# Performance work log

Measured on AMD Instinct MI355X. Metric: run time of the kernel, lower is better.

## Reference

```python
import jax, jax.numpy as jnp
import numpy as np

N = 50000      # total nodes (25 graphs x 2000 proteins)
E = 1200000    # total edges
G = 25         # graphs
F_IN = 128     # protein_features
H = 64         # hidden_dim
L = 2          # num_layers


def setup_inputs() -> dict:
    key = jax.random.key(0)
    ks = jax.random.split(key, 24)
    inp = {
        "x": jax.random.normal(ks[0], (N, F_IN), dtype=jnp.float32),
        "edge_attr": jax.random.uniform(ks[1], (E,), dtype=jnp.float32),
        "global_features": jax.random.normal(ks[2], (G, 6), dtype=jnp.float32),
        "edge_index": jax.random.randint(ks[3], (2, E), 0, N, dtype=jnp.int64),
        "batch": (jnp.arange(N, dtype=jnp.int64) // (N // G)),
    }
    s = 0.05
    inp["W_embed"] = jax.random.normal(ks[4], (F_IN, H), dtype=jnp.float32) * s
    inp["b_embed"] = jnp.zeros((H,), dtype=jnp.float32)
    inp["W_glob"] = jax.random.normal(ks[5], (6, H), dtype=jnp.float32) * s
    inp["b_glob"] = jnp.zeros((H,), dtype=jnp.float32)
    # stacked per-layer GATConv params (heads=1)
    inp["lin_W"] = jax.random.normal(ks[6], (L, H, H), dtype=jnp.float32) * s
    inp["att_src"] = jax.random.normal(ks[7], (L, H), dtype=jnp.float32) * s
    inp["att_dst"] = jax.random.normal(ks[8], (L, H), dtype=jnp.float32) * s
    inp["lin_edge_W"] = jax.random.normal(ks[9], (L, 1, H), dtype=jnp.float32) * s
    inp["att_edge"] = jax.random.normal(ks[10], (L, H), dtype=jnp.float32) * s
    inp["gat_bias"] = jnp.zeros((L, H), dtype=jnp.float32)
    inp["W_comb"] = jax.random.normal(ks[11], (2 * H, H), dtype=jnp.float32) * s
    inp["b_comb"] = jnp.zeros((H,), dtype=jnp.float32)
    inp["W_out"] = jax.random.normal(ks[12], (H, 1), dtype=jnp.float32) * s
    inp["b_out"] = jnp.zeros((1,), dtype=jnp.float32)
    return inp


def _forward(x, edge_attr, global_features, W_embed, b_embed, W_glob, b_glob,
             lin_W, att_src, att_dst, lin_edge_W, att_edge, gat_bias,
             W_comb, b_comb, W_out, b_out, edge_index, batch):
    src, dst = edge_index[0], edge_index[1]
    h = x @ W_embed + b_embed                       # [N,H]
    g = global_features @ W_glob + b_glob           # [G,H]
    ea = edge_attr[:, None]                         # [E,1] (edge_attr.unsqueeze(1))
    for l in range(L):
        hs = h @ lin_W[l]                           # [N,H] shared lin_src/lin_dst
        a_src = hs @ att_src[l]                     # [N]
        a_dst = hs @ att_dst[l]                     # [N]
        ef = ea @ lin_edge_W[l]                     # [E,H]
        a_edge = ef @ att_edge[l]                   # [E]
        alpha = jax.nn.leaky_relu(a_src[src] + a_dst[dst] + a_edge, 0.2)
        # segment softmax over incoming edges of each dst node
        m = jax.ops.segment_max(alpha, dst, num_segments=N)
        ex = jnp.exp(alpha - m[dst])
        denom = jax.ops.segment_sum(ex, dst, num_segments=N)
        alpha = ex / (denom[dst] + 1e-16)
        msg = alpha[:, None] * hs[src]              # [E,H]
        h = jax.ops.segment_sum(msg, dst, num_segments=N) + gat_bias[l]
        h = jax.nn.relu(h)
    # global_mean_pool
    counts = jax.ops.segment_sum(jnp.ones((N,), h.dtype), batch, num_segments=G)
    graph = jax.ops.segment_sum(h, batch, num_segments=G) / counts[:, None]
    combined = jax.nn.relu(jnp.concatenate([graph, g], axis=1) @ W_comb + b_comb)
    return combined @ W_out + b_out                 # [G,1]


def reference(x, edge_attr, global_features, W_embed, b_embed, W_glob, b_glob,
              lin_W, att_src, att_dst, lin_edge_W, att_edge, gat_bias,
              W_comb, b_comb, W_out, b_out, edge_index, batch):
    return _forward(x, edge_attr, global_features, W_embed, b_embed, W_glob, b_glob,
                    lin_W, att_src, att_dst, lin_edge_W, att_edge, gat_bias,
                    W_comb, b_comb, W_out, b_out, edge_index, batch)
```

## Files before the change

kernel.cpp:

```cpp
#include <hip/hip_runtime.h>
#include <hip/hip_fp16.h>
#include <math.h>

#define N_NODES 50000
#define N_EDGES 1200000
#define N_GRAPH 25
#define F_IN 128
#define H_DIM 64
#define NODES_PER_GRAPH 2000
#define POOL_CHUNKS 32

#define NBUCK 196
#define BUCK_CAP 8000
#define EPB 4096
#define NB_BIN ((N_EDGES + EPB - 1) / EPB)
#define NB_GEMM ((N_NODES + 63) / 64)

#define OFF_H     0
#define OFF_HS    (N_NODES*64)
#define OFF_ASRC  (OFF_HS + N_NODES*64)
#define OFF_ADST  (OFF_ASRC + N_NODES)
#define OFF_CBUF  (OFF_ADST + N_NODES)
#define OFF_BCUR  (OFF_CBUF + 16)
#define OFF_GSUM  (OFF_BCUR + 256)
#define OFF_ROWP  (OFF_GSUM + N_GRAPH*64)
#define OFF_ESRT  (OFF_ROWP + N_NODES + 2)

__global__ __launch_bounds__(256) void k_embed(const float* __restrict__ x,
                                               const float* __restrict__ W,
                                               const float* __restrict__ b,
                                               float* __restrict__ h,
                                               const float* __restrict__ linE,
                                               const float* __restrict__ attE,
                                               float* __restrict__ cbuf,
                                               int* __restrict__ bcur,
                                               float* __restrict__ gsum) {
    __shared__ float4 sW4[F_IN * 16];
    __shared__ float4 sx4[64 * 17];
    int tid = threadIdx.x;
    if (blockIdx.x == 0) {
        for (int i = tid; i < 256; i += 256) bcur[i] = 0;
        for (int i = tid; i < N_GRAPH * 64; i += 256) gsum[i] = 0.f;
        if (tid < 128) {
            int l = tid >> 6, j = tid & 63;
            float v = linE[l * 64 + j] * attE[l * 64 + j];
            #pragma unroll
            for (int m = 1; m < 64; m <<= 1) v += __shfl_xor(v, m);
            if (j == 0) cbuf[l] = v;
        }
    }
    int n0 = blockIdx.x * 64;
    const float4* W4 = (const float4*)W;
    const float4* x4 = (const float4*)x;
    #pragma unroll
    for (int i = 0; i < 8; ++i) sW4[tid + i * 256] = W4[tid + i * 256];

    int c4 = tid & 15, ng = tid >> 4;
    int r = tid >> 4, q = tid & 15;
    float4 acc[4];
    #pragma unroll
    for (int j = 0; j < 4; ++j) acc[j] = make_float4(0.f, 0.f, 0.f, 0.f);

    for (int kh = 0; kh < 2; ++kh) {
        __syncthreads();
        #pragma unroll
        for (int rb = 0; rb < 4; ++rb) {
            int rr = r + rb * 16;
            int n = n0 + rr;
            float4 v = make_float4(0.f, 0.f, 0.f, 0.f);
            if (n < N_NODES) v = x4[(size_t)n * 32 + kh * 16 + q];
            sx4[rr * 17 + q] = v;
        }
        __syncthreads();
        #pragma unroll
        for (int kq = 0; kq < 16; ++kq) {
            float4 wv[4];
            #pragma unroll
            for (int kk = 0; kk < 4; ++kk) wv[kk] = sW4[(kh * 64 + kq * 4 + kk) * 16 + c4];
            #pragma unroll
            for (int j = 0; j < 4; ++j) {
                float4 xv = sx4[(ng * 4 + j) * 17 + kq];
                float xs[4] = {xv.x, xv.y, xv.z, xv.w};
                #pragma unroll
                for (int kk = 0; kk < 4; ++kk) {
                    acc[j].x = fmaf(xs[kk], wv[kk].x, acc[j].x);
                    acc[j].y = fmaf(xs[kk], wv[kk].y, acc[j].y);
                    acc[j].z = fmaf(xs[kk], wv[kk].z, acc[j].z);
                    acc[j].w = fmaf(xs[kk], wv[kk].w, acc[j].w);
                }
            }
        }
    }
    float4 bb = ((const float4*)b)[c4];
    #pragma unroll
    for (int j = 0; j < 4; ++j) {
        int n = n0 + ng * 4 + j;
        if (n < N_NODES) {
            float4 v;
            v.x = acc[j].x + bb.x; v.y = acc[j].y + bb.y;
            v.z = acc[j].z + bb.z; v.w = acc[j].w + bb.w;
            ((float4*)h)[(size_t)n * 16 + c4] = v;
        }
    }
}

__global__ __launch_bounds__(256) void k_hs(const float* __restrict__ hin,
                                            const float* __restrict__ W,
                                            const float* __restrict__ attS,
                                            const float* __restrict__ attD,
                                            __half* __restrict__ hs_h,
                                            float* __restrict__ asrc,
                                            float* __restrict__ adst) {
    __shared__ float4 sW4[H_DIM * 16];
    __shared__ float4 sx4[64 * 17];
    int tid = threadIdx.x;
    int n0 = blockIdx.x * 64;
    const float4* W4 = (const float4*)W;
    const float4* h4 = (const float4*)hin;
    #pragma unroll
    for (int i = 0; i < 4; ++i) sW4[tid + i * 256] = W4[tid + i * 256];
    int r = tid >> 4, q = tid & 15;
    #pragma unroll
    for (int rb = 0; rb < 4; ++rb) {
        int rr = r + rb * 16;
        int n = n0 + rr;
        float4 v = make_float4(0.f, 0.f, 0.f, 0.f);
        if (n < N_NODES) v = h4[(size_t)n * 16 + q];
        sx4[rr * 17 + q] = v;
    }
    __syncthreads();

    int c4 = tid & 15, ng = tid >> 4;
    float4 acc[4];
    #pragma unroll
    for (int j = 0; j < 4; ++j) acc[j] = make_float4(0.f, 0.f, 0.f, 0.f);
    #pragma unroll
    for (int kq = 0; kq < 16; ++kq) {
        float4 wv[4];
        #pragma unroll
        for (int kk = 0; kk < 4; ++kk) wv[kk] = sW4[(kq * 4 + kk) * 16 + c4];
        #pragma unroll
        for (int j = 0; j < 4; ++j) {
            float4 xv = sx4[(ng * 4 + j) * 17 + kq];
            float xs[4] = {xv.x, xv.y, xv.z, xv.w};
            #pragma unroll
            for (int kk = 0; kk < 4; ++kk) {
                acc[j].x = fmaf(xs[kk], wv[kk].x, acc[j].x);
                acc[j].y = fmaf(xs[kk], wv[kk].y, acc[j].y);
                acc[j].z = fmaf(xs[kk], wv[kk].z, acc[j].z);
                acc[j].w = fmaf(xs[kk], wv[kk].w, acc[j].w);
            }
        }
    }
    float4 aS = ((const float4*)attS)[c4];
    float4 aD = ((const float4*)attD)[c4];
    #pragma unroll
    for (int j = 0; j < 4; ++j) {
        int n = n0 + ng * 4 + j;
        float rs = acc[j].x * aS.x + acc[j].y * aS.y + acc[j].z * aS.z + acc[j].w * aS.w;
        float rd = acc[j].x * aD.x + acc[j].y * aD.y + acc[j].z * aD.z + acc[j].w * aD.w;
        #pragma unroll
        for (int o = 1; o < 16; o <<= 1) {
            rs += __shfl_xor(rs, o);
            rd += __shfl_xor(rd, o);
        }
        if (n < N_NODES) {
            __half2 p0 = __floats2half2_rn(acc[j].x, acc[j].y);
            __half2 p1 = __floats2half2_rn(acc[j].z, acc[j].w);
            uint2 st;
            st.x = *(unsigned*)&p0;
            st.y = *(unsigned*)&p1;
            ((uint2*)hs_h)[(size_t)n * 16 + c4] = st;
            if (c4 == 0) { asrc[n] = rs; adst[n] = rd; }
        }
    }
}

__device__ __forceinline__ int block_excl_scan(int v, int tid, int* lds, int* total) {
    int lane = tid & 63, w = tid >> 6;
    int incl = v;
    #pragma unroll
    for (int off = 1; off < 64; off <<= 1) {
        int t = __shfl_up(incl, off);
        if (lane >= off) incl += t;
    }
    if (lane == 63) lds[w] = incl;
    __syncthreads();
    int wo = 0;
    for (int i = 0; i < w; ++i) wo += lds[i];
    *total = lds[0] + lds[1] + lds[2] + lds[3];
    __syncthreads();
    return wo + incl - v;
}

__global__ __launch_bounds__(256) void k_bin(const int* __restrict__ ei,
                                             const float* __restrict__ ea,
                                             uint2* __restrict__ stage,
                                             int* __restrict__ bcur) {
    __shared__ int lcnt[NBUCK];
    __shared__ int lbase[NBUCK];
    int tid = threadIdx.x;
    for (int i = tid; i < NBUCK; i += 256) lcnt[i] = 0;
    __syncthreads();
    int e0 = blockIdx.x * EPB;
    unsigned pw0[16], pw1[16];
    #pragma unroll
    for (int k = 0; k < 16; ++k) {
        int e = e0 + k * 256 + tid;
        bool ok = e < N_EDGES;
        int s = ok ? ei[e] : 0;
        int d = ok ? ei[N_EDGES + e] : 0;
        float v = ok ? ea[e] : 0.f;
        pw0[k] = (unsigned)s | ((unsigned)d << 16);
        pw1[k] = __float_as_uint(v);
        if (ok) atomicAdd(&lcnt[d >> 8], 1);
    }
    __syncthreads();
    for (int i = tid; i < NBUCK; i += 256) {
        lbase[i] = atomicAdd(&bcur[i], lcnt[i]);
        lcnt[i] = 0;
    }
    __syncthreads();
    #pragma unroll
    for (int k = 0; k < 16; ++k) {
        int e = e0 + k * 256 + tid;
        if (e < N_EDGES) {
            int b = pw0[k] >> 24;
            int pos = lbase[b] + atomicAdd(&lcnt[b], 1);
            uint2 t; t.x = pw0[k]; t.y = pw1[k];
            stage[b * BUCK_CAP + pos] = t;
        }
    }
}

__global__ __launch_bounds__(256) void k_group(const uint2* __restrict__ stage,
                                               const int* __restrict__ bcur,
                                               int* __restrict__ rowp,
                                               unsigned* __restrict__ esrt) {
    int b = blockIdx.x;
    int tid = threadIdx.x;
    __shared__ int sprefix[256];
    __shared__ int lcnt[256];
    __shared__ int lofs[256];
    __shared__ int slds[4];
    int bv = (tid < NBUCK) ? bcur[tid] : 0;
    int total;
    int bex = block_excl_scan(bv, tid, slds, &total);
    sprefix[tid] = bex;
    lcnt[tid] = 0;
    __syncthreads();
    int base = sprefix[b];
    int cntb = bcur[b];
    const uint2* reg = stage + b * BUCK_CAP;
    for (int i = tid; i < cntb; i += 256)
        atomicAdd(&lcnt[(reg[i].x >> 16) & 255], 1);
    __syncthreads();
    int ex = block_excl_scan(lcnt[tid], tid, slds, &total);
    lofs[tid] = base + ex;
    int n = b * 256 + tid;
    if (n < N_NODES) rowp[n] = base + ex;
    if (b == 0 && tid == 0) rowp[N_NODES] = N_EDGES;
    __syncthreads();
    lcnt[tid] = 0;
    __syncthreads();
    for (int i = tid; i < cntb; i += 256) {
        uint2 v = reg[i];
        int dloc = (v.x >> 16) & 255;
        int pos = lofs[dloc] + atomicAdd(&lcnt[dloc], 1);
        esrt[pos] = (v.x & 0xFFFFu) | ((v.y + 0x8000u) & 0xFFFF0000u);
    }
}

__global__ __launch_bounds__(256) void k_fused(const int* __restrict__ rowp,
                                               const unsigned* __restrict__ esrt,
                                               const float* __restrict__ asrc,
                                               const float* __restrict__ adst,
                                               const __half* __restrict__ hs_h,
                                               const float* __restrict__ cbuf,
                                               int layer,
                                               const float* __restrict__ gbias,
                                               float* __restrict__ hout) {
    int wid = (blockIdx.x * 256 + threadIdx.x) >> 6;
    int lane = threadIdx.x & 63;
    if (wid >= N_NODES) return;
    int beg = rowp[wid], end = rowp[wid + 1];
    float adv = adst[wid];
    float c = cbuf[layer];
    float m = -INFINITY, sum = 0.f;
    float acc[8];
    #pragma unroll
    for (int j = 0; j < 8; ++j) acc[j] = 0.f;
    int g8 = lane >> 3, fl8 = lane & 7;
    const uint4* hsq = (const uint4*)hs_h;

#define UNPACK_FMA(w_, r_)                                                      \
    {                                                                           \
        __half2 h0_ = *(__half2*)&r_.x, h1_ = *(__half2*)&r_.y;                 \
        __half2 h2_ = *(__half2*)&r_.z, h3_ = *(__half2*)&r_.w;                 \
        float2 f0_ = __half22float2(h0_), f1_ = __half22float2(h1_);            \
        float2 f2_ = __half22float2(h2_), f3_ = __half22float2(h3_);            \
        acc[0] = fmaf(w_, f0_.x, acc[0]); acc[1] = fmaf(w_, f0_.y, acc[1]);     \
        acc[2] = fmaf(w_, f1_.x, acc[2]); acc[3] = fmaf(w_, f1_.y, acc[3]);     \
        acc[4] = fmaf(w_, f2_.x, acc[4]); acc[5] = fmaf(w_, f2_.y, acc[5]);     \
        acc[6] = fmaf(w_, f3_.x, acc[6]); acc[7] = fmaf(w_, f3_.y, acc[7]);     \
    }

    for (int base = beg; base < end; base += 64) {
        int idx = base + lane;
        bool ok = idx < end;
        unsigned v = ok ? esrt[idx] : 0u;
        int s = v & 0xFFFF;
        float a;
        if (ok) {
            float eav = __uint_as_float(v & 0xFFFF0000u);
            a = asrc[s] + adv + c * eav;
            a = a >= 0.f ? a : 0.2f * a;
        } else {
            a = -INFINITY;
        }
        float cm = a;
        #pragma unroll
        for (int o = 1; o < 64; o <<= 1) cm = fmaxf(cm, __shfl_xor(cm, o));
        float newm = fmaxf(m, cm);
        float scale = __expf(m - newm);
        sum *= scale;
        #pragma unroll
        for (int j = 0; j < 8; ++j) acc[j] *= scale;
        m = newm;
        float ex = ok ? __expf(a - m) : 0.f;
        float cs = ex;
        #pragma unroll
        for (int o = 1; o < 64; o <<= 1) cs += __shfl_xor(cs, o);
        sum += cs;

        int lim = end - base; if (lim > 64) lim = 64;
        int t = g8;
        for (; t + 24 < lim; t += 32) {
            float w0 = __shfl(ex, t),      w1 = __shfl(ex, t + 8);
            float w2 = __shfl(ex, t + 16), w3 = __shfl(ex, t + 24);
            int   s0 = __shfl(s, t),       s1 = __shfl(s, t + 8);
            int   s2 = __shfl(s, t + 16),  s3 = __shfl(s, t + 24);
            uint4 r0 = hsq[s0 * 8 + fl8];
            uint4 r1 = hsq[s1 * 8 + fl8];
            uint4 r2 = hsq[s2 * 8 + fl8];
            uint4 r3 = hsq[s3 * 8 + fl8];
            UNPACK_FMA(w0, r0);
            UNPACK_FMA(w1, r1);
            UNPACK_FMA(w2, r2);
            UNPACK_FMA(w3, r3);
        }
        for (; t < lim; t += 8) {
            float w0 = __shfl(ex, t);
            int   s0 = __shfl(s, t);
            uint4 r0 = hsq[s0 * 8 + fl8];
            UNPACK_FMA(w0, r0);
        }
    }
#undef UNPACK_FMA
    #pragma unroll
    for (int o = 8; o < 64; o <<= 1) {
        #pragma unroll
        for (int j = 0; j < 8; ++j) acc[j] += __shfl_xor(acc[j], o);
    }

    if (lane < 8) {
        float inv = 1.f / (sum + 1e-16f);
        const float* gb = gbias + layer * H_DIM + lane * 8;
        float* op = hout + (size_t)wid * H_DIM + lane * 8;
        float4 v0, v1;
        v0.x = acc[0] * inv + gb[0]; v0.x = v0.x > 0.f ? v0.x : 0.f;
        v0.y = acc[1] * inv + gb[1]; v0.y = v0.y > 0.f ? v0.y : 0.f;
        v0.z = acc[2] * inv + gb[2]; v0.z = v0.z > 0.f ? v0.z : 0.f;
        v0.w = acc[3] * inv + gb[3]; v0.w = v0.w > 0.f ? v0.w : 0.f;
        v1.x = acc[4] * inv + gb[4]; v1.x = v1.x > 0.f ? v1.x : 0.f;
        v1.y = acc[5] * inv + gb[5]; v1.y = v1.y > 0.f ? v1.y : 0.f;
        v1.z = acc[6] * inv + gb[6]; v1.z = v1.z > 0.f ? v1.z : 0.f;
        v1.w = acc[7] * inv + gb[7]; v1.w = v1.w > 0.f ? v1.w : 0.f;
        ((float4*)op)[0] = v0;
        ((float4*)op)[1] = v1;
    }
}

__global__ __launch_bounds__(256) void k_pool(const float* __restrict__ h,
                                              float* __restrict__ gsum) {
    int g = blockIdx.x / POOL_CHUNKS;
    int chunk = blockIdx.x % POOL_CHUNKS;
    int wave = threadIdx.x >> 6, lane = threadIdx.x & 63;
    const int per_chunk = (NODES_PER_GRAPH + POOL_CHUNKS - 1) / POOL_CHUNKS;
    int n0 = g * NODES_PER_GRAPH + chunk * per_chunk;
    int n1 = g * NODES_PER_GRAPH + min((chunk + 1) * per_chunk, NODES_PER_GRAPH);
    float sum = 0.f;
    for (int n = n0 + wave; n < n1; n += 4)
        sum += h[(size_t)n * H_DIM + lane];
    __shared__ float spart[4][64];
    spart[wave][lane] = sum;
    __syncthreads();
    if (wave == 0) {
        float tot = spart[0][lane] + spart[1][lane] + spart[2][lane] + spart[3][lane];
        atomicAdd(gsum + g * H_DIM + lane, tot);
    }
}

__global__ __launch_bounds__(64) void k_head2(const float* __restrict__ gsum,
                                              const float* __restrict__ gf,
                                              const float* __restrict__ Wg,
                                              const float* __restrict__ bg,
                                              const float* __restrict__ Wc,
                                              const float* __restrict__ bc,
                                              const float* __restrict__ Wo,
                                              const float* __restrict__ bo,
                                              float* __restrict__ out) {
    int g = blockIdx.x;
    int lane = threadIdx.x;
    __shared__ float sgraph[64];
    __shared__ float sgf[64];
    sgraph[lane] = gsum[g * H_DIM + lane] / (float)NODES_PER_GRAPH;
    float gv = bg[lane];
    #pragma unroll
    for (int k = 0; k < 6; ++k) gv += gf[g * 6 + k] * Wg[k * 64 + lane];
    sgf[lane] = gv;
    __syncthreads();
    float cj = bc[lane];
    #pragma unroll
    for (int k = 0; k < 64; ++k) cj += sgraph[k] * Wc[k * 64 + lane];
    #pragma unroll
    for (int k = 0; k < 64; ++k) cj += sgf[k] * Wc[(64 + k) * 64 + lane];
    cj = cj > 0.f ? cj : 0.f;
    float o = cj * Wo[lane];
    #pragma unroll
    for (int m = 1; m < 64; m <<= 1) o += __shfl_xor(o, m);
    if (lane == 0) out[g] = o + bo[0];
}

extern "C" void kernel_launch(void* const* d_in, const int* in_sizes, int n_in,
                              void* d_out, int out_size, void* d_ws, size_t ws_size,
                              hipStream_t stream) {
    const float* x        = (const float*)d_in[0];
    const float* ea       = (const float*)d_in[1];
    const float* gf       = (const float*)d_in[2];
    const int*   ei       = (const int*)d_in[3];
    const float* W_embed  = (const float*)d_in[5];
    const float* b_embed  = (const float*)d_in[6];
    const float* W_glob   = (const float*)d_in[7];
    const float* b_glob   = (const float*)d_in[8];
    const float* lin_W    = (const float*)d_in[9];
    const float* att_src  = (const float*)d_in[10];
    const float* att_dst  = (const float*)d_in[11];
    const float* lin_eW   = (const float*)d_in[12];
    const float* att_edge = (const float*)d_in[13];
    const float* gat_bias = (const float*)d_in[14];
    const float* W_comb   = (const float*)d_in[15];
    const float* b_comb   = (const float*)d_in[16];
    const float* W_out    = (const float*)d_in[17];
    const float* b_out    = (const float*)d_in[18];
    float* out = (float*)d_out;
    float* ws  = (float*)d_ws;

    float*    h      = ws + OFF_H;
    __half*   hs_h   = (__half*)(ws + OFF_HS);
    uint2*    stage  = (uint2*)(ws + OFF_HS);
    float*    asrc   = ws + OFF_ASRC;
    float*    adst   = ws + OFF_ADST;
    float*    cbuf   = ws + OFF_CBUF;
    int*      bcur   = (int*)(ws + OFF_BCUR);
    float*    gsum   = ws + OFF_GSUM;
    int*      rowp   = (int*)(ws + OFF_ROWP);
    unsigned* esrt   = (unsigned*)(ws + OFF_ESRT);

    k_embed<<<NB_GEMM, 256, 0, stream>>>(x, W_embed, b_embed, h,
                                         lin_eW, att_edge, cbuf, bcur, gsum);

    k_bin<<<NB_BIN, 256, 0, stream>>>(ei, ea, stage, bcur);
    k_group<<<NBUCK, 256, 0, stream>>>(stage, bcur, rowp, esrt);

    for (int l = 0; l < 2; ++l) {
        k_hs<<<NB_GEMM, 256, 0, stream>>>(h, lin_W + l * 64 * 64,
                                          att_src + l * 64, att_dst + l * 64,
                                          hs_h, asrc, adst);
        k_fused<<<(N_NODES + 3) / 4, 256, 0, stream>>>(rowp, esrt,
                                                       asrc, adst, hs_h, cbuf, l,
                                                       gat_bias, h);
    }

    k_pool<<<N_GRAPH * POOL_CHUNKS, 256, 0, stream>>>(h, gsum);
    k_head2<<<N_GRAPH, 64, 0, stream>>>(gsum, gf, W_glob, b_glob,
                                        W_comb, b_comb, W_out, b_out, out);
}
```

Baseline: 202.7 us.

## Precompute per-edge source logits and process two nodes per wavefront

Adds a per-edge kernel that gathers asrc[src] plus the edge-attribute term into a packed (logit, src) array before each aggregation. The fused softmax-aggregate kernel now splits each 64-lane wavefront into two 32-lane halves, each handling its own destination node. This is meant to take the random asrc gather off the aggregation kernel's critical path and to cut idle lanes for nodes with about 24 incoming edges. In exchange it adds an extra launch and roughly 19 MB of traffic per layer (read esrt, write and re-read the 8-byte el2 array). Each half gathers only four edges of feature rows per step instead of eight.

```diff
diff --git a/kernel.cpp b/kernel.cpp
--- a/kernel.cpp
+++ b/kernel.cpp
@@ -25,6 +25,7 @@
 #define OFF_GSUM  (OFF_BCUR + 256)
 #define OFF_ROWP  (OFF_GSUM + N_GRAPH*64)
 #define OFF_ESRT  (OFF_ROWP + N_NODES + 2)
+#define OFF_EL2   (OFF_ESRT + N_EDGES)
 
 __global__ __launch_bounds__(256) void k_embed(const float* __restrict__ x,
                                                const float* __restrict__ W,
@@ -176,6 +177,21 @@
     }
 }
 
+__global__ __launch_bounds__(256) void k_el(const unsigned* __restrict__ esrt,
+                                            const float* __restrict__ asrc,
+                                            const float* __restrict__ cbuf,
+                                            int layer,
+                                            uint2* __restrict__ el2) {
+    int e = blockIdx.x * 256 + threadIdx.x;
+    if (e >= N_EDGES) return;
+    unsigned v = esrt[e];
+    unsigned s = v & 0xFFFFu;
+    float eav = __uint_as_float(v & 0xFFFF0000u);
+    float lg = asrc[s] + cbuf[layer] * eav;
+    uint2 r; r.x = __float_as_uint(lg); r.y = s;
+    el2[e] = r;
+}
+
 __device__ __forceinline__ int block_excl_scan(int v, int tid, int* lds, int* total) {
     int lane = tid & 63, w = tid >> 6;
     int incl = v;
@@ -272,25 +288,26 @@
 }
 
 __global__ __launch_bounds__(256) void k_fused(const int* __restrict__ rowp,
-                                               const unsigned* __restrict__ esrt,
-                                               const float* __restrict__ asrc,
+                                               const uint2* __restrict__ el2,
                                                const float* __restrict__ adst,
                                                const __half* __restrict__ hs_h,
-                                               const float* __restrict__ cbuf,
                                                int layer,
                                                const float* __restrict__ gbias,
                                                float* __restrict__ hout) {
-    int wid = (blockIdx.x * 256 + threadIdx.x) >> 6;
+    int pair = (blockIdx.x * 256 + threadIdx.x) >> 6;
     int lane = threadIdx.x & 63;
+    int half = lane >> 5, l32 = lane & 31;
+    int wid = pair * 2 + half;
     if (wid >= N_NODES) return;
     int beg = rowp[wid], end = rowp[wid + 1];
     float adv = adst[wid];
-    float c = cbuf[layer];
     float m = -INFINITY, sum = 0.f;
     float acc[8];
     #pragma unroll
     for (int j = 0; j < 8; ++j) acc[j] = 0.f;
-    int g8 = lane >> 3, fl8 = lane & 7;
+    int g = (lane >> 3) & 3;
+    int fl8 = lane & 7;
+    int hb = half * 32;
     const uint4* hsq = (const uint4*)hs_h;
 
 #define UNPACK_FMA(w_, r_)                                                      \
@@ -305,22 +322,22 @@
         acc[6] = fmaf(w_, f3_.x, acc[6]); acc[7] = fmaf(w_, f3_.y, acc[7]);     \
     }
 
-    for (int base = beg; base < end; base += 64) {
-        int idx = base + lane;
+    for (int base = beg; base < end; base += 32) {
+        int idx = base + l32;
         bool ok = idx < end;
-        unsigned v = ok ? esrt[idx] : 0u;
-        int s = v & 0xFFFF;
         float a;
+        int s = 0;
         if (ok) {
-            float eav = __uint_as_float(v & 0xFFFF0000u);
-            a = asrc[s] + adv + c * eav;
+            uint2 v = el2[idx];
+            s = (int)v.y;
+            a = __uint_as_float(v.x) + adv;
             a = a >= 0.f ? a : 0.2f * a;
         } else {
             a = -INFINITY;
         }
         float cm = a;
         #pragma unroll
-        for (int o = 1; o < 64; o <<= 1) cm = fmaxf(cm, __shfl_xor(cm, o));
+        for (int o = 1; o < 32; o <<= 1) cm = fmaxf(cm, __shfl_xor(cm, o));
         float newm = fmaxf(m, cm);
         float scale = __expf(m - newm);
         sum *= scale;
@@ -330,16 +347,16 @@
         float ex = ok ? __expf(a - m) : 0.f;
         float cs = ex;
         #pragma unroll
-        for (int o = 1; o < 64; o <<= 1) cs += __shfl_xor(cs, o);
+        for (int o = 1; o < 32; o <<= 1) cs += __shfl_xor(cs, o);
         sum += cs;
 
-        int lim = end - base; if (lim > 64) lim = 64;
-        int t = g8;
-        for (; t + 24 < lim; t += 32) {
-            float w0 = __shfl(ex, t),      w1 = __shfl(ex, t + 8);
-            float w2 = __shfl(ex, t + 16), w3 = __shfl(ex, t + 24);
-            int   s0 = __shfl(s, t),       s1 = __shfl(s, t + 8);
-            int   s2 = __shfl(s, t + 16),  s3 = __shfl(s, t + 24);
+        int lim = end - base; if (lim > 32) lim = 32;
+        int t = g;
+        for (; t + 12 < lim; t += 16) {
+            float w0 = __shfl(ex, hb + t),      w1 = __shfl(ex, hb + t + 4);
+            float w2 = __shfl(ex, hb + t + 8),  w3 = __shfl(ex, hb + t + 12);
+            int   s0 = __shfl(s, hb + t),       s1 = __shfl(s, hb + t + 4);
+            int   s2 = __shfl(s, hb + t + 8),   s3 = __shfl(s, hb + t + 12);
             uint4 r0 = hsq[s0 * 8 + fl8];
             uint4 r1 = hsq[s1 * 8 + fl8];
             uint4 r2 = hsq[s2 * 8 + fl8];
@@ -349,24 +366,24 @@
             UNPACK_FMA(w2, r2);
             UNPACK_FMA(w3, r3);
         }
-        for (; t < lim; t += 8) {
-            float w0 = __shfl(ex, t);
-            int   s0 = __shfl(s, t);
+        for (; t < lim; t += 4) {
+            float w0 = __shfl(ex, hb + t);
+            int   s0 = __shfl(s, hb + t);
             uint4 r0 = hsq[s0 * 8 + fl8];
             UNPACK_FMA(w0, r0);
         }
     }
 #undef UNPACK_FMA
     #pragma unroll
-    for (int o = 8; o < 64; o <<= 1) {
+    for (int o = 8; o < 32; o <<= 1) {
         #pragma unroll
         for (int j = 0; j < 8; ++j) acc[j] += __shfl_xor(acc[j], o);
     }
 
-    if (lane < 8) {
+    if (l32 < 8) {
         float inv = 1.f / (sum + 1e-16f);
-        const float* gb = gbias + layer * H_DIM + lane * 8;
-        float* op = hout + (size_t)wid * H_DIM + lane * 8;
+        const float* gb = gbias + layer * H_DIM + l32 * 8;
+        float* op = hout + (size_t)wid * H_DIM + l32 * 8;
         float4 v0, v1;
         v0.x = acc[0] * inv + gb[0]; v0.x = v0.x > 0.f ? v0.x : 0.f;
         v0.y = acc[1] * inv + gb[1]; v0.y = v0.y > 0.f ? v0.y : 0.f;
@@ -466,20 +483,23 @@
     float*    gsum   = ws + OFF_GSUM;
     int*      rowp   = (int*)(ws + OFF_ROWP);
     unsigned* esrt   = (unsigned*)(ws + OFF_ESRT);
+    uint2*    el2    = (uint2*)(ws + OFF_EL2);
 
     k_embed<<<NB_GEMM, 256, 0, stream>>>(x, W_embed, b_embed, h,
                                          lin_eW, att_edge, cbuf, bcur, gsum);
 
     k_bin<<<NB_BIN, 256, 0, stream>>>(ei, ea, stage, bcur);
     k_group<<<NBUCK, 256, 0, stream>>>(stage, bcur, rowp, esrt);
+
+    const int egrid = (N_EDGES + 255) / 256;
+    const int fgrid = (N_NODES / 2 + 3) / 4;
 
     for (int l = 0; l < 2; ++l) {
         k_hs<<<NB_GEMM, 256, 0, stream>>>(h, lin_W + l * 64 * 64,
                                           att_src + l * 64, att_dst + l * 64,
                                           hs_h, asrc, adst);
-        k_fused<<<(N_NODES + 3) / 4, 256, 0, stream>>>(rowp, esrt,
-                                                       asrc, adst, hs_h, cbuf, l,
-                                                       gat_bias, h);
+        k_el<<<egrid, 256, 0, stream>>>(esrt, asrc, cbuf, l, el2);
+        k_fused<<<fgrid, 256, 0, stream>>>(rowp, el2, adst, hs_h, l, gat_bias, h);
     }
 
     k_pool<<<N_GRAPH * POOL_CHUNKS, 256, 0, stream>>>(h, gsum);
```

New measurement: 192.8 us. 1.05x faster.
